# Kernel optimization log

Hardware: AMD Instinct MI355X
Metric: run time of the kernel (lower is better)

## Reference

```python
import jax, jax.numpy as jnp
import numpy as np

EMB = 1024
HEADS = 16
HEAD_DIM = EMB // HEADS


def setup_inputs() -> dict:
    key = jax.random.key(0)
    ks = jax.random.split(key, 9)
    s = 1.0 / np.sqrt(EMB)  # torch Linear default init scale (uniform), use normal*s for simplicity of magnitude
    x = jax.random.normal(ks[0], (2, 2048, EMB), dtype=jnp.float32)
    wQ = jax.random.uniform(ks[1], (EMB, EMB), jnp.float32, -s, s)
    bQ = jax.random.uniform(ks[2], (EMB,), jnp.float32, -s, s)
    wK = jax.random.uniform(ks[3], (EMB, EMB), jnp.float32, -s, s)
    bK = jax.random.uniform(ks[4], (EMB,), jnp.float32, -s, s)
    wV = jax.random.uniform(ks[5], (EMB, EMB), jnp.float32, -s, s)
    bV = jax.random.uniform(ks[6], (EMB,), jnp.float32, -s, s)
    wO = jax.random.uniform(ks[7], (EMB, EMB), jnp.float32, -s, s)
    bO = jax.random.uniform(ks[8], (EMB,), jnp.float32, -s, s)
    return {"x": x, "wQ": wQ, "bQ": bQ, "wK": wK, "bK": bK, "wV": wV, "bV": bV, "wO": wO, "bO": bO}


def reference(x, wQ, bQ, wK, bK, wV, bV, wO, bO):
    B, S, E = x.shape
    H, Dh = HEADS, HEAD_DIM
    # manual LayerNorm-like scaling; torch.std uses unbiased (ddof=1)
    mu = jnp.mean(x, axis=-1, keepdims=True)
    sd = jnp.std(x, axis=-1, keepdims=True, ddof=1)
    xn = (x - mu) / (sd + 1e-6)
    # torch Linear: y = x @ W.T + b
    q = (xn @ wQ.T + bQ).reshape(B, S, H, Dh).transpose(0, 2, 1, 3)  # [B,H,S,Dh]
    k = (xn @ wK.T + bK).reshape(B, S, H, Dh).transpose(0, 2, 1, 3)
    v = (xn @ wV.T + bV).reshape(B, S, H, Dh).transpose(0, 2, 1, 3)
    scores = jnp.einsum('bhsd,bhtd->bhst', q, k) / np.sqrt(Dh).astype(np.float32)
    A = jax.nn.softmax(scores, axis=-1)
    Hout = jnp.einsum('bhst,bhtd->bhsd', A, v)  # [B,H,S,Dh]
    Hout = Hout.transpose(0, 2, 1, 3).reshape(B, S, E)
    return Hout @ wO.T + bO
```

## Files before the change

### kernel.cpp

```cpp
#include <hip/hip_runtime.h>
#include <cstdint>
#include <cstddef>

typedef __bf16 bf16x8 __attribute__((ext_vector_type(8)));
typedef float f32x4 __attribute__((ext_vector_type(4)));
typedef unsigned short us4 __attribute__((ext_vector_type(4)));
typedef unsigned short us8 __attribute__((ext_vector_type(8)));
typedef unsigned int ui4 __attribute__((ext_vector_type(4)));
typedef unsigned short u16;

#define QSCALE 0.18033688011112042f

#define MFMA16(a, b, c) __builtin_amdgcn_mfma_f32_16x16x32_bf16((a), (b), (c), 0, 0, 0)
#define GLOAD16(g, l)                                                        \
  __builtin_amdgcn_global_load_lds(                                          \
      (const __attribute__((address_space(1))) void*)(g),                    \
      (__attribute__((address_space(3))) void*)(l), 16, 0, 0)

__device__ __forceinline__ u16 f2bf(float x) {
  unsigned int u = __float_as_uint(x);
  unsigned int r = u + 0x7fffu + ((u >> 16) & 1u);
  return (u16)(r >> 16);
}

__global__ __launch_bounds__(256) void prep_kernel(
    const float* __restrict__ x, const float* __restrict__ wq,
    const float* __restrict__ wk, const float* __restrict__ wv,
    const float* __restrict__ wo, u16* __restrict__ xn,
    u16* __restrict__ wdst) {
  const int bid = blockIdx.x;
  const int t = threadIdx.x;
  if (bid < 4096) {
    const int row = bid;
    const float* xr = x + (size_t)row * 1024;
    float4 v = *(const float4*)(xr + t * 4);
    float s = v.x + v.y + v.z + v.w;
    float s2 = v.x * v.x + v.y * v.y + v.z * v.z + v.w * v.w;
#pragma unroll
    for (int o = 32; o >= 1; o >>= 1) {
      s += __shfl_xor(s, o);
      s2 += __shfl_xor(s2, o);
    }
    __shared__ float red[8];
    const int wv_ = t >> 6, ln = t & 63;
    if (ln == 0) {
      red[wv_] = s;
      red[4 + wv_] = s2;
    }
    __syncthreads();
    s = red[0] + red[1] + red[2] + red[3];
    s2 = red[4] + red[5] + red[6] + red[7];
    const float mu = s * (1.0f / 1024.0f);
    float var = (s2 - 1024.0f * mu * mu) * (1.0f / 1023.0f);
    var = fmaxf(var, 0.0f);
    const float inv = 1.0f / (sqrtf(var) + 1e-6f);
    us4 o;
    o.x = f2bf((v.x - mu) * inv);
    o.y = f2bf((v.y - mu) * inv);
    o.z = f2bf((v.z - mu) * inv);
    o.w = f2bf((v.w - mu) * inv);
    *(us4*)(xn + (size_t)row * 1024 + t * 4) = o;
  } else {
    const int wid = bid - 4096;
    const int mat = wid >> 9, xi = wid & 511;
    const float* src = (mat == 0) ? wq : (mat == 1) ? wk : (mat == 2) ? wv : wo;
    const float sc = (mat == 0) ? QSCALE : 1.0f;
    u16* d = wdst + ((size_t)mat << 20);
    const size_t i = ((size_t)xi * 256 + t) * 8;
    float4 a = *(const float4*)(src + i);
    float4 b = *(const float4*)(src + i + 4);
    us8 o;
    o[0] = f2bf(a.x * sc);
    o[1] = f2bf(a.y * sc);
    o[2] = f2bf(a.z * sc);
    o[3] = f2bf(a.w * sc);
    o[4] = f2bf(b.x * sc);
    o[5] = f2bf(b.y * sc);
    o[6] = f2bf(b.z * sc);
    o[7] = f2bf(b.w * sc);
    *(us8*)(d + i) = o;
  }
}

__device__ __forceinline__ void gemm64_core(const u16* __restrict__ A,
                                            const u16* __restrict__ W,
                                            int m0, int n0,
                                            u16 (*As)[64 * 32],
                                            u16 (*Bs)[128 * 32],
                                            f32x4 acc[2][4]) {
  const int tid = threadIdx.x;
  const int lane = tid & 63, wave = tid >> 6;
  const int wm = wave >> 1, wn = wave & 1;
  const int lr = lane & 15, lg = lane >> 4;

  auto stage = [&](int buf, int kt) {
    {
      const int row = tid >> 2, ch = tid & 3;
      const int sc = ch ^ ((row >> 1) & 3);
      GLOAD16(A + (size_t)(m0 + row) * 1024 + kt * 32 + sc * 8,
              &As[buf][tid * 8]);
    }
#pragma unroll
    for (int i = 0; i < 2; i++) {
      const int idx = i * 256 + tid;
      const int row = idx >> 2, ch = idx & 3;
      const int sc = ch ^ ((row >> 1) & 3);
      GLOAD16(W + (size_t)(n0 + row) * 1024 + kt * 32 + sc * 8,
              &Bs[buf][idx * 8]);
    }
  };

  stage(0, 0);
  const int cs = (lg ^ ((lr >> 1) & 3)) * 8;
  int cur = 0;
  for (int kt = 0; kt < 32; ++kt) {
    __syncthreads();
    if (kt + 1 < 32) stage(cur ^ 1, kt + 1);
    bf16x8 af[2], bfr[4];
#pragma unroll
    for (int m = 0; m < 2; m++)
      af[m] = *(const bf16x8*)&As[cur][(wm * 32 + m * 16 + lr) * 32 + cs];
#pragma unroll
    for (int n = 0; n < 4; n++)
      bfr[n] = *(const bf16x8*)&Bs[cur][(wn * 64 + n * 16 + lr) * 32 + cs];
#pragma unroll
    for (int m = 0; m < 2; m++)
#pragma unroll
      for (int n = 0; n < 4; n++)
        acc[m][n] = MFMA16(af[m], bfr[n], acc[m][n]);
    cur ^= 1;
  }
}

__global__ __launch_bounds__(256, 5) void qkv_gemm(
    const u16* __restrict__ xn, const u16* __restrict__ Wall,
    const float* __restrict__ bQ, const float* __restrict__ bK,
    const float* __restrict__ bV, u16* __restrict__ Qb, u16* __restrict__ Kb,
    u16* __restrict__ VTb) {
  __shared__ u16 As[2][64 * 32];
  __shared__ u16 Bs[2][128 * 32];
  const int z = blockIdx.z;
  const u16* W = Wall + ((size_t)z << 20);
  const float* bias = (z == 0) ? bQ : (z == 1) ? bK : bV;
  const float bscale = (z == 0) ? QSCALE : 1.0f;
  const int m0 = blockIdx.x * 64, n0 = blockIdx.y * 128;
  f32x4 acc[2][4] = {};
  gemm64_core(xn, W, m0, n0, As, Bs, acc);

  const int lane = threadIdx.x & 63, wave = threadIdx.x >> 6;
  const int wm = wave >> 1, wn = wave & 1, lr = lane & 15, lg = lane >> 4;
  if (z == 2) {
#pragma unroll
    for (int n = 0; n < 4; n++) {
      const int col = n0 + wn * 64 + n * 16 + lr;
      const float bv = bias[col];
      const int hh = col >> 6, d = col & 63;
#pragma unroll
      for (int m = 0; m < 2; m++) {
        const int rb = m0 + wm * 32 + m * 16 + lg * 4;
#pragma unroll
        for (int j = 0; j < 4; j++) {
          const int row = rb + j;
          const int bb = row >> 11, s = row & 2047;
          VTb[(((size_t)(bb * 16 + hh) * 64 + d) << 11) + s] =
              f2bf(acc[m][n][j] + bv);
        }
      }
    }
  } else {
    u16* o = (z == 0) ? Qb : Kb;
#pragma unroll
    for (int n = 0; n < 4; n++) {
      const int col = n0 + wn * 64 + n * 16 + lr;
      const float bv = bias[col] * bscale;
#pragma unroll
      for (int m = 0; m < 2; m++) {
        const int rb = m0 + wm * 32 + m * 16 + lg * 4;
#pragma unroll
        for (int j = 0; j < 4; j++)
          o[(size_t)(rb + j) * 1024 + col] = f2bf(acc[m][n][j] + bv);
      }
    }
  }
}

__global__ __launch_bounds__(256, 5) void o_gemm(const u16* __restrict__ A,
                                                 const u16* __restrict__ W,
                                                 const float* __restrict__ bias,
                                                 float* __restrict__ out) {
  __shared__ u16 As[2][64 * 32];
  __shared__ u16 Bs[2][128 * 32];
  const int m0 = blockIdx.x * 64, n0 = blockIdx.y * 128;
  f32x4 acc[2][4] = {};
  gemm64_core(A, W, m0, n0, As, Bs, acc);
  const int lane = threadIdx.x & 63, wave = threadIdx.x >> 6;
  const int wm = wave >> 1, wn = wave & 1, lr = lane & 15, lg = lane >> 4;
#pragma unroll
  for (int n = 0; n < 4; n++) {
    const int col = n0 + wn * 64 + n * 16 + lr;
    const float bv = bias[col];
#pragma unroll
    for (int m = 0; m < 2; m++) {
      const int rb = m0 + wm * 32 + m * 16 + lg * 4;
#pragma unroll
      for (int j = 0; j < 4; j++)
        out[(size_t)(rb + j) * 1024 + col] = acc[m][n][j] + bv;
    }
  }
}

__global__ __launch_bounds__(256, 2) void attn_kernel(
    const u16* __restrict__ Qb, const u16* __restrict__ Kb,
    const u16* __restrict__ VTb, u16* __restrict__ Hb) {
  __shared__ u16 Ks[2][128 * 64];
  __shared__ u16 Vs[2][2][64 * 64];
  const int tid = threadIdx.x;
  const int wave = tid >> 6, lane = tid & 63;
  const int lr = lane & 15, lg = lane >> 4;
  const int qb = blockIdx.x, bh = blockIdx.y;
  const int b = bh >> 4, h = bh & 15;

  bf16x8 aq[2][2];
#pragma unroll
  for (int qg = 0; qg < 2; qg++) {
    const int qrow = b * 2048 + qb * 128 + wave * 32 + qg * 16 + lr;
    const u16* qsrc = Qb + (size_t)qrow * 1024 + h * 64 + lg * 8;
    aq[qg][0] = *(const bf16x8*)qsrc;
    aq[qg][1] = *(const bf16x8*)(qsrc + 32);
  }

  f32x4 oacc[2][4] = {};
  f32x4 lacc[2] = {};
  const ui4 ones_u = {0x3f803f80u, 0x3f803f80u, 0x3f803f80u, 0x3f803f80u};
  const bf16x8 ones = __builtin_bit_cast(bf16x8, ones_u);

  auto stage = [&](int buf, int kt) {
#pragma unroll
    for (int i = 0; i < 4; i++) {
      const int idx = i * 256 + tid;
      const int r = idx >> 3, c = idx & 7;
      GLOAD16(Kb + (size_t)(b * 2048 + kt * 128 + r) * 1024 + h * 64 +
                  (c ^ (r & 7)) * 8,
              &Ks[buf][idx * 8]);
    }
#pragma unroll
    for (int half = 0; half < 2; half++) {
#pragma unroll
      for (int i = 0; i < 2; i++) {
        const int jdx = i * 256 + tid;
        const int r = jdx >> 3, lc = jdx & 7;
        GLOAD16(VTb + (size_t)(bh * 64 + r) * 2048 + kt * 128 +
                    (half * 8 + (lc ^ (r & 7))) * 8,
                &Vs[buf][half][jdx * 8]);
      }
    }
  };

  auto softpack = [&](f32x4 (&s)[8], ui4 (&pf)[4]) {
#pragma unroll
    for (int n = 0; n < 8; n++)
#pragma unroll
      for (int j = 0; j < 4; j++)
        s[n][j] = __builtin_amdgcn_exp2f(s[n][j]);
    unsigned int w[8][2];
#pragma unroll
    for (int n = 0; n < 8; n++) {
      asm("v_cvt_pk_bf16_f32 %0, %1, %2"
          : "=v"(w[n][0])
          : "v"(s[n][0]), "v"(s[n][1]));
      asm("v_cvt_pk_bf16_f32 %0, %1, %2"
          : "=v"(w[n][1])
          : "v"(s[n][2]), "v"(s[n][3]));
    }
#pragma unroll
    for (int ks = 0; ks < 4; ks++) {
      unsigned int pw[4];
#pragma unroll
      for (int rp = 0; rp < 2; rp++) {
        unsigned int a = w[2 * ks][rp], bb = w[2 * ks + 1][rp];
        asm("v_permlane32_swap_b32 %0, %1" : "+v"(a), "+v"(bb));
        asm("v_permlane16_swap_b32 %0, %1" : "+v"(a), "+v"(bb));
        pw[rp] = a;
        pw[2 + rp] = bb;
      }
      pf[ks] = (ui4){pw[0], pw[1], pw[2], pw[3]};
    }
  };

  stage(0, 0);
  int cur = 0;
  for (int kt = 0; kt < 16; ++kt) {
    __syncthreads();
    if (kt + 1 < 16) stage(cur ^ 1, kt + 1);

    f32x4 s0[8], s1[8];
#pragma unroll
    for (int n = 0; n < 8; n++) {
      s0[n] = (f32x4){0.f, 0.f, 0.f, 0.f};
      s1[n] = (f32x4){0.f, 0.f, 0.f, 0.f};
    }
    __builtin_amdgcn_s_setprio(1);
#pragma unroll
    for (int n = 0; n < 8; n++) {
      const int row = n * 16 + lr;
#pragma unroll
      for (int ks = 0; ks < 2; ks++) {
        const int byo = (ks * 64 + lg * 16) ^ ((row & 7) << 4);
        const bf16x8 kfr = *(const bf16x8*)&Ks[cur][row * 64 + (byo >> 1)];
        s0[n] = MFMA16(kfr, aq[0][ks], s0[n]);
        s1[n] = MFMA16(kfr, aq[1][ks], s1[n]);
      }
    }
    __builtin_amdgcn_s_setprio(0);

    ui4 pf0[4], pf1[4];
    softpack(s0, pf0);
    softpack(s1, pf1);

    __builtin_amdgcn_s_setprio(1);
#pragma unroll
    for (int ks = 0; ks < 4; ks++) {
      const int half = ks >> 1, ks2 = ks & 1;
      const bf16x8 p0 = __builtin_bit_cast(bf16x8, pf0[ks]);
      const bf16x8 p1 = __builtin_bit_cast(bf16x8, pf1[ks]);
#pragma unroll
      for (int n = 0; n < 4; n++) {
        const int row = n * 16 + lr;
        const int ch = ((ks2 * 4 + lg) ^ (row & 7)) * 8;
        const bf16x8 vb = *(const bf16x8*)&Vs[cur][half][row * 64 + ch];
        oacc[0][n] = MFMA16(p0, vb, oacc[0][n]);
        oacc[1][n] = MFMA16(p1, vb, oacc[1][n]);
      }
      lacc[0] = MFMA16(p0, ones, lacc[0]);
      lacc[1] = MFMA16(p1, ones, lacc[1]);
    }
    __builtin_amdgcn_s_setprio(0);
    cur ^= 1;
  }

#pragma unroll
  for (int qg = 0; qg < 2; qg++) {
    float rl[4];
#pragma unroll
    for (int j = 0; j < 4; j++) rl[j] = 1.0f / lacc[qg][j];
    const int hrow_base = b * 2048 + qb * 128 + wave * 32 + qg * 16 + lg * 4;
#pragma unroll
    for (int n = 0; n < 4; n++) {
      const int col = h * 64 + n * 16 + lr;
#pragma unroll
      for (int j = 0; j < 4; j++) {
        const float val = oacc[qg][n][j] * rl[j];
        Hb[(size_t)(hrow_base + j) * 1024 + col] = f2bf(val);
      }
    }
  }
}

extern "C" void kernel_launch(void* const* d_in, const int* in_sizes, int n_in,
                              void* d_out, int out_size, void* d_ws,
                              size_t ws_size, hipStream_t stream) {
  const float* x = (const float*)d_in[0];
  const float* wQ = (const float*)d_in[1];
  const float* bQ = (const float*)d_in[2];
  const float* wK = (const float*)d_in[3];
  const float* bK = (const float*)d_in[4];
  const float* wV = (const float*)d_in[5];
  const float* bV = (const float*)d_in[6];
  const float* wO = (const float*)d_in[7];
  const float* bO = (const float*)d_in[8];
  float* out = (float*)d_out;

  char* ws = (char*)d_ws;
  u16* xn = (u16*)(ws);
  u16* Wall = (u16*)(ws + ((size_t)8 << 20));
  u16* Qb = (u16*)(ws + ((size_t)16 << 20));
  u16* Kb = (u16*)(ws + ((size_t)24 << 20));
  u16* VTb = (u16*)(ws + ((size_t)32 << 20));
  u16* Hb = (u16*)(ws + ((size_t)40 << 20));

  prep_kernel<<<6144, 256, 0, stream>>>(x, wQ, wK, wV, wO, xn, Wall);
  qkv_gemm<<<dim3(64, 8, 3), 256, 0, stream>>>(xn, Wall, bQ, bK, bV, Qb, Kb,
                                               VTb);
  attn_kernel<<<dim3(16, 32), 256, 0, stream>>>(Qb, Kb, VTb, Hb);
  o_gemm<<<dim3(64, 8), 256, 0, stream>>>(Hb, Wall + ((size_t)3 << 20), bO,
                                          out);
}
```

Measured before the change: 118.7 us.

## Double GEMM K-tile to 64 and give each attention wave 64 query rows

The shared GEMM core now stages 64-wide K tiles with an XOR swizzle on 8-element chunks, which halves the number of barrier iterations per block. The attention kernel processes 256 query rows per block (64 per wave, four 16-row groups), so each staged K/V tile is reused across twice as many queries and the grid is halved. The cost is more LDS and registers per block; launch bounds drop to 3 and 1 blocks per CU, and only 256 attention blocks are launched, which may leave compute units underused.

```diff
diff --git a/kernel.cpp b/kernel.cpp
--- a/kernel.cpp
+++ b/kernel.cpp
@@ -82,70 +82,73 @@
   }
 }
 
-__device__ __forceinline__ void gemm64_core(const u16* __restrict__ A,
-                                            const u16* __restrict__ W,
-                                            int m0, int n0,
-                                            u16 (*As)[64 * 32],
-                                            u16 (*Bs)[128 * 32],
-                                            f32x4 acc[2][4]) {
+__device__ __forceinline__ void gemm64k64_core(const u16* __restrict__ A,
+                                               const u16* __restrict__ W,
+                                               int m0, int n0,
+                                               u16 (*As)[64 * 64],
+                                               u16 (*Bs)[128 * 64],
+                                               f32x4 acc[2][4]) {
   const int tid = threadIdx.x;
   const int lane = tid & 63, wave = tid >> 6;
   const int wm = wave >> 1, wn = wave & 1;
   const int lr = lane & 15, lg = lane >> 4;
 
   auto stage = [&](int buf, int kt) {
-    {
-      const int row = tid >> 2, ch = tid & 3;
-      const int sc = ch ^ ((row >> 1) & 3);
-      GLOAD16(A + (size_t)(m0 + row) * 1024 + kt * 32 + sc * 8,
-              &As[buf][tid * 8]);
-    }
 #pragma unroll
     for (int i = 0; i < 2; i++) {
       const int idx = i * 256 + tid;
-      const int row = idx >> 2, ch = idx & 3;
-      const int sc = ch ^ ((row >> 1) & 3);
-      GLOAD16(W + (size_t)(n0 + row) * 1024 + kt * 32 + sc * 8,
+      const int r = idx >> 3, c = idx & 7;
+      GLOAD16(A + (size_t)(m0 + r) * 1024 + kt * 64 + (c ^ (r & 7)) * 8,
+              &As[buf][idx * 8]);
+    }
+#pragma unroll
+    for (int i = 0; i < 4; i++) {
+      const int idx = i * 256 + tid;
+      const int r = idx >> 3, c = idx & 7;
+      GLOAD16(W + (size_t)(n0 + r) * 1024 + kt * 64 + (c ^ (r & 7)) * 8,
               &Bs[buf][idx * 8]);
     }
   };
 
   stage(0, 0);
-  const int cs = (lg ^ ((lr >> 1) & 3)) * 8;
   int cur = 0;
-  for (int kt = 0; kt < 32; ++kt) {
+  for (int kt = 0; kt < 16; ++kt) {
     __syncthreads();
-    if (kt + 1 < 32) stage(cur ^ 1, kt + 1);
-    bf16x8 af[2], bfr[4];
-#pragma unroll
-    for (int m = 0; m < 2; m++)
-      af[m] = *(const bf16x8*)&As[cur][(wm * 32 + m * 16 + lr) * 32 + cs];
-#pragma unroll
-    for (int n = 0; n < 4; n++)
-      bfr[n] = *(const bf16x8*)&Bs[cur][(wn * 64 + n * 16 + lr) * 32 + cs];
-#pragma unroll
-    for (int m = 0; m < 2; m++)
+    if (kt + 1 < 16) stage(cur ^ 1, kt + 1);
+#pragma unroll
+    for (int ks = 0; ks < 2; ks++) {
+      const int co = ((ks * 4 + lg) ^ (lr & 7)) * 8;
+      bf16x8 af[2], bfr[4];
+#pragma unroll
+      for (int m = 0; m < 2; m++)
+        af[m] = *(const bf16x8*)&As[cur][(wm * 32 + m * 16 + lr) * 64 + co];
 #pragma unroll
       for (int n = 0; n < 4; n++)
-        acc[m][n] = MFMA16(af[m], bfr[n], acc[m][n]);
+        bfr[n] = *(const bf16x8*)&Bs[cur][(wn * 64 + n * 16 + lr) * 64 + co];
+#pragma unroll
+      for (int m = 0; m < 2; m++)
+#pragma unroll
+        for (int n = 0; n < 4; n++)
+          acc[m][n] = MFMA16(af[m], bfr[n], acc[m][n]);
+    }
     cur ^= 1;
   }
 }
 
-__global__ __launch_bounds__(256, 5) void qkv_gemm(
+__global__ __launch_bounds__(256, 3) void qkv_gemm(
     const u16* __restrict__ xn, const u16* __restrict__ Wall,
     const float* __restrict__ bQ, const float* __restrict__ bK,
     const float* __restrict__ bV, u16* __restrict__ Qb, u16* __restrict__ Kb,
     u16* __restrict__ VTb) {
-  __shared__ u16 As[2][64 * 32];
-  __shared__ u16 Bs[2][128 * 32];
+  __shared__ u16 As[2][64 * 64];
+  __shared__ u16 Bs[2][128 * 64];
   const int z = blockIdx.z;
   const u16* W = Wall + ((size_t)z << 20);
   const float* bias = (z == 0) ? bQ : (z == 1) ? bK : bV;
   const float bscale = (z == 0) ? QSCALE : 1.0f;
   const int m0 = blockIdx.x * 64, n0 = blockIdx.y * 128;
   f32x4 acc[2][4] = {};
-  gemm64_core(xn, W, m0, n0, As, Bs, acc);
+  gemm64k64_core(xn, W, m0, n0, As, Bs, acc);
 
   const int lane = threadIdx.x & 63, wave = threadIdx.x >> 6;
   const int wm = wave >> 1, wn = wave & 1, lr = lane & 15, lg = lane >> 4;
@@ -184,15 +187,15 @@
   }
 }
 
-__global__ __launch_bounds__(256, 5) void o_gemm(const u16* __restrict__ A,
+__global__ __launch_bounds__(256, 3) void o_gemm(const u16* __restrict__ A,
                                                  const u16* __restrict__ W,
                                                  const float* __restrict__ bias,
                                                  float* __restrict__ out) {
-  __shared__ u16 As[2][64 * 32];
-  __shared__ u16 Bs[2][128 * 32];
+  __shared__ u16 As[2][64 * 64];
+  __shared__ u16 Bs[2][128 * 64];
   const int m0 = blockIdx.x * 64, n0 = blockIdx.y * 128;
   f32x4 acc[2][4] = {};
-  gemm64_core(A, W, m0, n0, As, Bs, acc);
+  gemm64k64_core(A, W, m0, n0, As, Bs, acc);
   const int lane = threadIdx.x & 63, wave = threadIdx.x >> 6;
   const int wm = wave >> 1, wn = wave & 1, lr = lane & 15, lg = lane >> 4;
 #pragma unroll
@@ -209,7 +212,7 @@
   }
 }
 
-__global__ __launch_bounds__(256, 2) void attn_kernel(
+__global__ __launch_bounds__(256, 1) void attn_kernel(
     const u16* __restrict__ Qb, const u16* __restrict__ Kb,
     const u16* __restrict__ VTb, u16* __restrict__ Hb) {
   __shared__ u16 Ks[2][128 * 64];
@@ -220,17 +223,17 @@
   const int qb = blockIdx.x, bh = blockIdx.y;
   const int b = bh >> 4, h = bh & 15;
 
-  bf16x8 aq[2][2];
-#pragma unroll
-  for (int qg = 0; qg < 2; qg++) {
-    const int qrow = b * 2048 + qb * 128 + wave * 32 + qg * 16 + lr;
+  bf16x8 aq[4][2];
+#pragma unroll
+  for (int qg = 0; qg < 4; qg++) {
+    const int qrow = b * 2048 + qb * 256 + wave * 64 + qg * 16 + lr;
     const u16* qsrc = Qb + (size_t)qrow * 1024 + h * 64 + lg * 8;
     aq[qg][0] = *(const bf16x8*)qsrc;
     aq[qg][1] = *(const bf16x8*)(qsrc + 32);
   }
 
-  f32x4 oacc[2][4] = {};
-  f32x4 lacc[2] = {};
+  f32x4 oacc[4][4] = {};
+  f32x4 lacc[4] = {};
   const ui4 ones_u = {0x3f803f80u, 0x3f803f80u, 0x3f803f80u, 0x3f803f80u};
   const bf16x8 ones = __builtin_bit_cast(bf16x8, ones_u);
 
@@ -293,11 +296,13 @@
     __syncthreads();
     if (kt + 1 < 16) stage(cur ^ 1, kt + 1);
 
-    f32x4 s0[8], s1[8];
+    f32x4 s0[8], s1[8], s2[8], s3[8];
 #pragma unroll
     for (int n = 0; n < 8; n++) {
       s0[n] = (f32x4){0.f, 0.f, 0.f, 0.f};
       s1[n] = (f32x4){0.f, 0.f, 0.f, 0.f};
+      s2[n] = (f32x4){0.f, 0.f, 0.f, 0.f};
+      s3[n] = (f32x4){0.f, 0.f, 0.f, 0.f};
     }
     __builtin_amdgcn_s_setprio(1);
 #pragma unroll
@@ -309,13 +314,17 @@
         const bf16x8 kfr = *(const bf16x8*)&Ks[cur][row * 64 + (byo >> 1)];
         s0[n] = MFMA16(kfr, aq[0][ks], s0[n]);
         s1[n] = MFMA16(kfr, aq[1][ks], s1[n]);
+        s2[n] = MFMA16(kfr, aq[2][ks], s2[n]);
+        s3[n] = MFMA16(kfr, aq[3][ks], s3[n]);
       }
     }
     __builtin_amdgcn_s_setprio(0);
 
-    ui4 pf0[4], pf1[4];
+    ui4 pf0[4], pf1[4], pf2[4], pf3[4];
     softpack(s0, pf0);
     softpack(s1, pf1);
+    softpack(s2, pf2);
+    softpack(s3, pf3);
 
     __builtin_amdgcn_s_setprio(1);
 #pragma unroll
@@ -323,6 +332,8 @@
       const int half = ks >> 1, ks2 = ks & 1;
       const bf16x8 p0 = __builtin_bit_cast(bf16x8, pf0[ks]);
       const bf16x8 p1 = __builtin_bit_cast(bf16x8, pf1[ks]);
+      const bf16x8 p2 = __builtin_bit_cast(bf16x8, pf2[ks]);
+      const bf16x8 p3 = __builtin_bit_cast(bf16x8, pf3[ks]);
 #pragma unroll
       for (int n = 0; n < 4; n++) {
         const int row = n * 16 + lr;
@@ -330,20 +341,24 @@
         const bf16x8 vb = *(const bf16x8*)&Vs[cur][half][row * 64 + ch];
         oacc[0][n] = MFMA16(p0, vb, oacc[0][n]);
         oacc[1][n] = MFMA16(p1, vb, oacc[1][n]);
+        oacc[2][n] = MFMA16(p2, vb, oacc[2][n]);
+        oacc[3][n] = MFMA16(p3, vb, oacc[3][n]);
       }
       lacc[0] = MFMA16(p0, ones, lacc[0]);
       lacc[1] = MFMA16(p1, ones, lacc[1]);
+      lacc[2] = MFMA16(p2, ones, lacc[2]);
+      lacc[3] = MFMA16(p3, ones, lacc[3]);
     }
     __builtin_amdgcn_s_setprio(0);
     cur ^= 1;
   }
 
 #pragma unroll
-  for (int qg = 0; qg < 2; qg++) {
+  for (int qg = 0; qg < 4; qg++) {
     float rl[4];
 #pragma unroll
     for (int j = 0; j < 4; j++) rl[j] = 1.0f / lacc[qg][j];
-    const int hrow_base = b * 2048 + qb * 128 + wave * 32 + qg * 16 + lg * 4;
+    const int hrow_base = b * 2048 + qb * 256 + wave * 64 + qg * 16 + lg * 4;
 #pragma unroll
     for (int n = 0; n < 4; n++) {
       const int col = h * 64 + n * 16 + lr;
@@ -381,7 +396,7 @@
   prep_kernel<<<6144, 256, 0, stream>>>(x, wQ, wK, wV, wO, xn, Wall);
   qkv_gemm<<<dim3(64, 8, 3), 256, 0, stream>>>(xn, Wall, bQ, bK, bV, Qb, Kb,
                                                VTb);
-  attn_kernel<<<dim3(16, 32), 256, 0, stream>>>(Qb, Kb, VTb, Hb);
+  attn_kernel<<<dim3(8, 32), 256, 0, stream>>>(Qb, Kb, VTb, Hb);
   o_gemm<<<dim3(64, 8), 256, 0, stream>>>(Hb, Wall + ((size_t)3 << 20), bO,
                                           out);
 }
```

Measured after the change: 121.9 us. 2.7% more time.
